# Performance work log

Hardware: AMD Instinct MI355X
Metric: run time of the kernel (lower is better)

Reference implementation:

```python
import jax, jax.numpy as jnp
import numpy as np

D_MODEL = 2048
D_FF = 8192


def _act_quant(x):
    # BitNet b1.58 per-token int8 absmax activation quantization with STE passthrough
    scale = 127.0 / jnp.clip(jnp.max(jnp.abs(x), axis=-1, keepdims=True), 1e-5)
    xq = jnp.clip(jnp.round(x * scale), -128.0, 127.0) / scale
    return x + jax.lax.stop_gradient(xq - x)


def _weight_quant(w):
    # Ternary {-1,0,1} weight quantization with per-tensor mean-abs scale
    scale = 1.0 / jnp.clip(jnp.mean(jnp.abs(w)), 1e-5)
    wq = jnp.clip(jnp.round(w * scale), -1.0, 1.0) / scale
    return w + jax.lax.stop_gradient(wq - w)


def _bitlinear(x, w):
    # y = Q_act(x) @ Q_w(w)^T   (w has shape [out, in], torch Linear convention)
    return jnp.einsum('bsd,fd->bsf', _act_quant(x), _weight_quant(w))


def setup_inputs() -> dict:
    key = jax.random.key(0)
    k_x, k_w1, k_w2 = jax.random.split(key, 3)
    x = jax.random.normal(k_x, (4, 4096, D_MODEL), dtype=jnp.float32)
    # torch Linear default init scale ~ 1/sqrt(fan_in)
    W1 = jax.random.normal(k_w1, (D_FF, D_MODEL), dtype=jnp.float32) / np.sqrt(D_MODEL)
    W2 = jax.random.normal(k_w2, (D_MODEL, D_FF), dtype=jnp.float32) / np.sqrt(D_FF)
    return {"x": x, "W1": W1, "W2": W2}


def reference(x, W1, W2):
    h = jax.nn.silu(_bitlinear(x, W1))   # [B, S, d_ff]
    return _bitlinear(h, W2)             # [B, S, d_model]; dropout p=0 -> identity
```

## Files before the change

### kernel.cpp

```cpp
#include <hip/hip_runtime.h>
#include <hip/hip_bf16.h>
#include <cstdint>

#define DM 2048
#define DF 8192

typedef int v4i __attribute__((ext_vector_type(4)));
typedef short v8s __attribute__((ext_vector_type(8)));

__device__ __forceinline__ float silu_f(float y) {
  return y * (1.0f / (1.0f + expf(-y)));
}

__device__ __forceinline__ void gload_lds16(const void* g, void* l) {
  __builtin_amdgcn_global_load_lds(
      (const __attribute__((address_space(1))) void*)g,
      (__attribute__((address_space(3))) void*)l, 16, 0, 0);
}

__global__ __launch_bounds__(256) void abs_sum_k(const float* __restrict__ w,
                                                 float* __restrict__ partial) {
  const int t = threadIdx.x;
  const float4* wp = (const float4*)w;
  const long base = (long)blockIdx.x * 4096;
  float s = 0.f;
#pragma unroll
  for (int i = 0; i < 16; ++i) {
    float4 v = wp[base + i * 256 + t];
    s += fabsf(v.x) + fabsf(v.y) + fabsf(v.z) + fabsf(v.w);
  }
#pragma unroll
  for (int d = 1; d < 64; d <<= 1) s += __shfl_xor(s, d, 64);
  __shared__ float wsum[4];
  if ((t & 63) == 0) wsum[t >> 6] = s;
  __syncthreads();
  if (t == 0) partial[blockIdx.x] = (wsum[0] + wsum[1]) + (wsum[2] + wsum[3]);
}

__global__ __launch_bounds__(256) void finalize_scales_k(const float* __restrict__ p1,
                                                         const float* __restrict__ p2,
                                                         float* __restrict__ sc) {
  const float* p = (blockIdx.x == 0) ? p1 : p2;
  const int t = threadIdx.x;
  float s = (p[t] + p[t + 256]) + (p[t + 512] + p[t + 768]);
#pragma unroll
  for (int d = 1; d < 64; d <<= 1) s += __shfl_xor(s, d, 64);
  __shared__ float wsum[4];
  if ((t & 63) == 0) wsum[t >> 6] = s;
  __syncthreads();
  if (t == 0) {
    float total = (wsum[0] + wsum[1]) + (wsum[2] + wsum[3]);
    float mean = total * (1.0f / 16777216.0f);
    float c = fmaxf(mean, 1e-5f);
    sc[blockIdx.x * 2 + 0] = 1.0f / c;
    sc[blockIdx.x * 2 + 1] = c;
  }
}

__global__ __launch_bounds__(256) void tern_quant_k(const float* __restrict__ w,
                                                    int8_t* __restrict__ wq,
                                                    const float* __restrict__ scp) {
  const float s = scp[0];
  const long i = (long)blockIdx.x * 256 + threadIdx.x;
  float4 v = ((const float4*)w)[i];
  int q0 = (int)rintf(v.x * s); q0 = q0 < -1 ? -1 : (q0 > 1 ? 1 : q0);
  int q1 = (int)rintf(v.y * s); q1 = q1 < -1 ? -1 : (q1 > 1 ? 1 : q1);
  int q2 = (int)rintf(v.z * s); q2 = q2 < -1 ? -1 : (q2 > 1 ? 1 : q2);
  int q3 = (int)rintf(v.w * s); q3 = q3 < -1 ? -1 : (q3 > 1 ? 1 : q3);
  ((int*)wq)[i] = (q0 & 255) | ((q1 & 255) << 8) | ((q2 & 255) << 16) | ((q3 & 255) << 24);
}

__global__ __launch_bounds__(256) void act_quant_x_k(const float* __restrict__ x,
                                                     int8_t* __restrict__ xq,
                                                     float* __restrict__ inv_sx) {
  const int t = threadIdx.x;
  const long row = blockIdx.x;
  const float4* xr = (const float4*)(x + row * DM);
  float4 v0 = xr[t * 2], v1 = xr[t * 2 + 1];
  float m = fmaxf(fmaxf(fmaxf(fabsf(v0.x), fabsf(v0.y)), fmaxf(fabsf(v0.z), fabsf(v0.w))),
                  fmaxf(fmaxf(fabsf(v1.x), fabsf(v1.y)), fmaxf(fabsf(v1.z), fabsf(v1.w))));
#pragma unroll
  for (int d = 1; d < 64; d <<= 1) m = fmaxf(m, __shfl_xor(m, d, 64));
  __shared__ float wm[4];
  if ((t & 63) == 0) wm[t >> 6] = m;
  __syncthreads();
  m = fmaxf(fmaxf(wm[0], wm[1]), fmaxf(wm[2], wm[3]));
  const float scale = 127.0f / fmaxf(m, 1e-5f);
  if (t == 0) inv_sx[row] = 1.0f / scale;
  float vv[8] = {v0.x, v0.y, v0.z, v0.w, v1.x, v1.y, v1.z, v1.w};
  int q[8];
#pragma unroll
  for (int j = 0; j < 8; ++j) {
    int qq = (int)rintf(vv[j] * scale);
    q[j] = qq < -128 ? -128 : (qq > 127 ? 127 : qq);
  }
  int lo = (q[0] & 255) | ((q[1] & 255) << 8) | ((q[2] & 255) << 16) | ((q[3] & 255) << 24);
  int hi = (q[4] & 255) | ((q[5] & 255) << 8) | ((q[6] & 255) << 16) | ((q[7] & 255) << 24);
  ((int2*)(xq + row * DM))[t] = make_int2(lo, hi);
}

template <int MO, int NO>
__device__ __forceinline__ void cluster(const v4i (&af)[4][2], const v4i (&bf)[2][2],
                                        v4i (&acc)[8][4]) {
  __builtin_amdgcn_s_setprio(1);
#pragma unroll
  for (int ks = 0; ks < 2; ++ks)
#pragma unroll
    for (int m = 0; m < 4; ++m)
#pragma unroll
      for (int n = 0; n < 2; ++n)
        acc[MO + m][NO + n] = __builtin_amdgcn_mfma_i32_16x16x64_i8(
            af[m][ks], bf[n][ks], acc[MO + m][NO + n], 0, 0, 0);
  __builtin_amdgcn_s_setprio(0);
}

template <int K, int N, int EPI>
__global__ __launch_bounds__(512, 2) void gemm8_i8_k(
    const int8_t* __restrict__ A, const int8_t* __restrict__ B,
    const float* __restrict__ rowInv, const float* __restrict__ invswp,
    short* __restrict__ Y16, float* __restrict__ Out) {
  constexpr int NT = K / 128;
  constexpr int NBX = N / 256;
  __shared__ __align__(16) uint8_t lds[131072];

  const int t = threadIdx.x;
  const int wave = t >> 6;
  const int lane = t & 63;
  const int wr = wave >> 2;
  const int wc = wave & 3;
  const int l15 = lane & 15, l4 = lane >> 4;

  const int cpx = (int)gridDim.x >> 3;
  const int bid0 = blockIdx.x;
  const int bid = (bid0 & 7) * cpx + (bid0 >> 3);
  const int bx = bid % NBX, by = bid / NBX;
  const long arow0 = (long)by * 256;
  const long bcol0 = (long)bx * 256;

  const int8_t* Ablk = A + arow0 * K;
  const int8_t* Bblk = B + bcol0 * K;

  const int srow = t >> 3;
  const int scol = ((t & 7) ^ (srow & 7)) << 4;

  const int rAo = (wr * 128 + l15) * 128;
  const int rBo = (wc * 64 + l15) * 128;
  const int sw = (l15 & 7) << 4;
  const int cc0 = (l4 * 16) ^ sw;
  const int cc1 = (64 | (l4 * 16)) ^ sw;

  v4i acc[8][4] = {};
  v4i a_lo[4][2], a_hi[4][2], b_lo[2][2], b_hi[2][2];

#define STAGE(ktile_, part_)                                                      \
  do {                                                                            \
    const int kk = (ktile_);                                                      \
    if (kk < NT) {                                                                \
      uint8_t* d0 = lds + ((kk & 1) << 16) + ((part_) << 14) + (wave << 10);      \
      const int8_t* sp = ((part_) < 2) ? Ablk : Bblk;                             \
      const int8_t* s0 =                                                          \
          sp + (long)((((part_) & 1) << 7) + srow) * K + ((long)kk << 7) + scol;  \
      gload_lds16(s0, d0);                                                        \
      gload_lds16(s0 + ((long)K << 6), d0 + 8192);                                \
    }                                                                             \
  } while (0)

#define FENCE       asm volatile("" ::: "memory")
#define WAIT_LGKM0  asm volatile("s_waitcnt lgkmcnt(0)"  ::: "memory")
#define WAIT_VM4    asm volatile("s_waitcnt vmcnt(4)"    ::: "memory")
#define WAIT_VM0    asm volatile("s_waitcnt vmcnt(0)"    ::: "memory")

  STAGE(0, 0); STAGE(0, 1); STAGE(0, 2); STAGE(0, 3);
  STAGE(1, 0); STAGE(1, 1);
  WAIT_VM4;
  __builtin_amdgcn_s_barrier();
  FENCE;
  {
    const uint8_t* sA0 = lds;
#pragma unroll
    for (int m = 0; m < 4; ++m) {
      a_lo[m][0] = *(const v4i*)(sA0 + rAo + m * 2048 + cc0);
      a_lo[m][1] = *(const v4i*)(sA0 + rAo + m * 2048 + cc1);
    }
  }

  for (int kt = 0; kt < NT; ++kt) {
    const uint8_t* sA = lds + ((kt & 1) << 16);
    const uint8_t* sB = sA + 32768;
    const uint8_t* sAn = lds + (((kt + 1) & 1) << 16);

#pragma unroll
    for (int n = 0; n < 2; ++n) {
      b_lo[n][0] = *(const v4i*)(sB + rBo + n * 2048 + cc0);
      b_lo[n][1] = *(const v4i*)(sB + rBo + n * 2048 + cc1);
    }
#pragma unroll
    for (int n = 0; n < 2; ++n) {
      b_hi[n][0] = *(const v4i*)(sB + rBo + (n + 2) * 2048 + cc0);
      b_hi[n][1] = *(const v4i*)(sB + rBo + (n + 2) * 2048 + cc1);
    }
#pragma unroll
    for (int m = 0; m < 4; ++m) {
      a_hi[m][0] = *(const v4i*)(sA + rAo + (m + 4) * 2048 + cc0);
      a_hi[m][1] = *(const v4i*)(sA + rAo + (m + 4) * 2048 + cc1);
    }
    STAGE(kt + 1, 2);
    STAGE(kt + 1, 3);
    cluster<0, 0>(a_lo, b_lo, acc);
    cluster<0, 2>(a_lo, b_hi, acc);
    WAIT_VM4;
    WAIT_LGKM0;
    __builtin_amdgcn_s_barrier();
    FENCE;
    if (kt + 1 < NT) {
#pragma unroll
      for (int m = 0; m < 4; ++m) {
        a_lo[m][0] = *(const v4i*)(sAn + rAo + m * 2048 + cc0);
        a_lo[m][1] = *(const v4i*)(sAn + rAo + m * 2048 + cc1);
      }
    }
    STAGE(kt + 2, 0);
    STAGE(kt + 2, 1);
    cluster<4, 0>(a_hi, b_lo, acc);
    cluster<4, 2>(a_hi, b_hi, acc);
    if (kt < NT - 2) {
      WAIT_VM4;
    } else {
      WAIT_VM0;
    }
    __builtin_amdgcn_s_barrier();
    FENCE;
  }

  if constexpr (EPI == 1) {
    __syncthreads();
#pragma unroll
    for (int mi = 0; mi < 8; ++mi) {
#pragma unroll
      for (int r = 0; r < 4; ++r) {
        const int row = wr * 128 + mi * 16 + l4 * 4 + r;
#pragma unroll
        for (int ni = 0; ni < 4; ++ni) {
          int yi = acc[mi][ni][r];
          int ys = yi < -32767 ? -32767 : (yi > 32767 ? 32767 : yi);
          const int col = wc * 64 + ni * 16 + l15;
          *(short*)(lds + ((row * 512 + col * 2) ^ ((row & 7) << 4))) = (short)ys;
        }
      }
    }
    __syncthreads();
    const int row = t >> 1;
    const int half = t & 1;
    short* gp = Y16 + (arow0 + row) * (long)DF + bcol0 + half * 128;
#pragma unroll
    for (int i = 0; i < 16; ++i) {
      v8s yv = *(const v8s*)(lds + ((row * 512 + half * 256 + i * 16) ^ ((row & 7) << 4)));
      *(v8s*)(gp + i * 8) = yv;
    }
  } else {
    const float invsw = invswp[0];
#pragma unroll
    for (int mi = 0; mi < 8; ++mi) {
#pragma unroll
      for (int r = 0; r < 4; ++r) {
        const long grow = arow0 + wr * 128 + mi * 16 + l4 * 4 + r;
        const float c2 = rowInv[grow] * invsw;
#pragma unroll
        for (int ni = 0; ni < 4; ++ni)
          Out[grow * N + bcol0 + wc * 64 + ni * 16 + l15] = (float)acc[mi][ni][r] * c2;
      }
    }
  }
#undef STAGE
#undef FENCE
#undef WAIT_LGKM0
#undef WAIT_VM4
#undef WAIT_VM0
}

__global__ __launch_bounds__(256) void quant_h_k(const short* __restrict__ Y16,
                                                 const float* __restrict__ inv_sx,
                                                 const float* __restrict__ sc,
                                                 int8_t* __restrict__ hq,
                                                 float* __restrict__ inv_sh) {
  const int t = threadIdx.x;
  const long row = blockIdx.x;
  const float c1 = inv_sx[row] * sc[1];
  const v8s* yp = (const v8s*)(Y16 + row * DF);
  float h[32];
  float mx = 0.f;
#pragma unroll
  for (int b = 0; b < 4; ++b) {
    v8s s8 = yp[b * 256 + t];
#pragma unroll
    for (int j = 0; j < 8; ++j) {
      float hv = silu_f((float)s8[j] * c1);
      h[b * 8 + j] = hv;
      mx = fmaxf(mx, fabsf(hv));
    }
  }
#pragma unroll
  for (int d = 1; d < 64; d <<= 1) mx = fmaxf(mx, __shfl_xor(mx, d, 64));
  __shared__ float wm[4];
  if ((t & 63) == 0) wm[t >> 6] = mx;
  __syncthreads();
  const float m = fmaxf(fmaxf(wm[0], wm[1]), fmaxf(wm[2], wm[3]));
  const float scale = 127.0f / fmaxf(m, 1e-5f);
  if (t == 0) inv_sh[row] = 1.0f / scale;
  int2* op = (int2*)(hq + row * DF);
#pragma unroll
  for (int b = 0; b < 4; ++b) {
    int q[8];
#pragma unroll
    for (int j = 0; j < 8; ++j) {
      int qq = (int)rintf(h[b * 8 + j] * scale);
      q[j] = qq < -128 ? -128 : (qq > 127 ? 127 : qq);
    }
    int lo = (q[0] & 255) | ((q[1] & 255) << 8) | ((q[2] & 255) << 16) | ((q[3] & 255) << 24);
    int hi = (q[4] & 255) | ((q[5] & 255) << 8) | ((q[6] & 255) << 16) | ((q[7] & 255) << 24);
    op[b * 256 + t] = make_int2(lo, hi);
  }
}

extern "C" void kernel_launch(void* const* d_in, const int* in_sizes, int n_in,
                              void* d_out, int out_size, void* d_ws, size_t ws_size,
                              hipStream_t stream) {
  const float* x = (const float*)d_in[0];
  const float* W1 = (const float*)d_in[1];
  const float* W2 = (const float*)d_in[2];
  float* out = (float*)d_out;

  uint8_t* w = (uint8_t*)d_ws;
  float* sc = (float*)(w + 0);
  float* p1 = (float*)(w + 256);
  float* p2 = (float*)(w + 256 + 4096);
  float* inv_sx = (float*)(w + 8448);
  float* inv_sh = (float*)(w + 8448 + 65536);
  uint8_t* w1q = w + 8448 + 131072 + 4194304;
  uint8_t* w2q = w1q + 16777216;
  uint8_t* xq = w2q + 16777216;
  uint8_t* hq = xq + 33554432;
  short* y16 = (short*)(hq + 134217728);

  abs_sum_k<<<1024, 256, 0, stream>>>(W1, p1);
  abs_sum_k<<<1024, 256, 0, stream>>>(W2, p2);
  finalize_scales_k<<<2, 256, 0, stream>>>(p1, p2, sc);
  tern_quant_k<<<16384, 256, 0, stream>>>(W1, (int8_t*)w1q, sc + 0);
  tern_quant_k<<<16384, 256, 0, stream>>>(W2, (int8_t*)w2q, sc + 2);
  act_quant_x_k<<<16384, 256, 0, stream>>>(x, (int8_t*)xq, inv_sx);
  gemm8_i8_k<2048, 8192, 1><<<2048, 512, 0, stream>>>(
      (const int8_t*)xq, (const int8_t*)w1q, nullptr, nullptr, y16, nullptr);
  quant_h_k<<<16384, 256, 0, stream>>>(y16, inv_sx, sc, (int8_t*)hq, inv_sh);
  gemm8_i8_k<8192, 2048, 0><<<512, 512, 0, stream>>>(
      (const int8_t*)hq, (const int8_t*)w2q, inv_sh, sc + 3, nullptr, out);
}
```

Baseline: 765.2 us.

## Load B fragments directly from global into registers, stage only A in LDS

The int8 GEMM now stages only the A tile through LDS and has each wave load its B (weight) fragments straight from global memory into registers, prefetching the next k-tile during the MFMA clusters. Block ordering is flipped so consecutive blocks share the same B column tile, which favours cache reuse of the weights. The main loop has one barrier per k-tile instead of two and the vmcnt thresholds are adjusted to match. This removes LDS traffic and writes for B, at the cost of uncoalesced 16-byte global loads per lane and more register pressure.

```diff
diff --git a/kernel.cpp b/kernel.cpp
--- a/kernel.cpp
+++ b/kernel.cpp
@@ -115,12 +115,12 @@
 }
 
 template <int K, int N, int EPI>
-__global__ __launch_bounds__(512, 2) void gemm8_i8_k(
+__global__ __launch_bounds__(512, 2) void gemmbd_i8_k(
     const int8_t* __restrict__ A, const int8_t* __restrict__ B,
     const float* __restrict__ rowInv, const float* __restrict__ invswp,
     short* __restrict__ Y16, float* __restrict__ Out) {
   constexpr int NT = K / 128;
-  constexpr int NBX = N / 256;
+  constexpr int NBY = 64;
   __shared__ __align__(16) uint8_t lds[131072];
 
   const int t = threadIdx.x;
@@ -133,101 +133,93 @@
   const int cpx = (int)gridDim.x >> 3;
   const int bid0 = blockIdx.x;
   const int bid = (bid0 & 7) * cpx + (bid0 >> 3);
-  const int bx = bid % NBX, by = bid / NBX;
+  const int by = bid % NBY, bx = bid / NBY;
   const long arow0 = (long)by * 256;
   const long bcol0 = (long)bx * 256;
 
   const int8_t* Ablk = A + arow0 * K;
-  const int8_t* Bblk = B + bcol0 * K;
 
   const int srow = t >> 3;
   const int scol = ((t & 7) ^ (srow & 7)) << 4;
 
   const int rAo = (wr * 128 + l15) * 128;
-  const int rBo = (wc * 64 + l15) * 128;
   const int sw = (l15 & 7) << 4;
   const int cc0 = (l4 * 16) ^ sw;
   const int cc1 = (64 | (l4 * 16)) ^ sw;
 
+  const int8_t* Bfrag = B + (bcol0 + wc * 64 + l15) * (long)K + l4 * 16;
+
   v4i acc[8][4] = {};
   v4i a_lo[4][2], a_hi[4][2], b_lo[2][2], b_hi[2][2];
 
-#define STAGE(ktile_, part_)                                                      \
+#define STAGEA(ktile_, part_)                                                     \
   do {                                                                            \
     const int kk = (ktile_);                                                      \
     if (kk < NT) {                                                                \
-      uint8_t* d0 = lds + ((kk & 1) << 16) + ((part_) << 14) + (wave << 10);      \
-      const int8_t* sp = ((part_) < 2) ? Ablk : Bblk;                             \
+      uint8_t* d0 = lds + ((kk & 1) << 15) + ((part_) << 14) + (wave << 10);      \
       const int8_t* s0 =                                                          \
-          sp + (long)((((part_) & 1) << 7) + srow) * K + ((long)kk << 7) + scol;  \
+          Ablk + (long)(((part_) << 7) + srow) * K + ((long)kk << 7) + scol;      \
       gload_lds16(s0, d0);                                                        \
       gload_lds16(s0 + ((long)K << 6), d0 + 8192);                                \
     }                                                                             \
   } while (0)
 
+#define LOAD_BLO(kk_)                                                             \
+  _Pragma("unroll")                                                               \
+  for (int n = 0; n < 2; ++n) {                                                   \
+    b_lo[n][0] = *(const v4i*)(Bfrag + (long)n * 16 * K + ((long)(kk_) << 7));    \
+    b_lo[n][1] = *(const v4i*)(Bfrag + (long)n * 16 * K + ((long)(kk_) << 7) + 64); \
+  }
+
+#define LOAD_BHI(kk_)                                                             \
+  _Pragma("unroll")                                                               \
+  for (int n = 0; n < 2; ++n) {                                                   \
+    b_hi[n][0] = *(const v4i*)(Bfrag + (long)(n + 2) * 16 * K + ((long)(kk_) << 7)); \
+    b_hi[n][1] = *(const v4i*)(Bfrag + (long)(n + 2) * 16 * K + ((long)(kk_) << 7) + 64); \
+  }
+
 #define FENCE       asm volatile("" ::: "memory")
 #define WAIT_LGKM0  asm volatile("s_waitcnt lgkmcnt(0)"  ::: "memory")
-#define WAIT_VM4    asm volatile("s_waitcnt vmcnt(4)"    ::: "memory")
+#define WAIT_VM8    asm volatile("s_waitcnt vmcnt(8)"    ::: "memory")
 #define WAIT_VM0    asm volatile("s_waitcnt vmcnt(0)"    ::: "memory")
 
-  STAGE(0, 0); STAGE(0, 1); STAGE(0, 2); STAGE(0, 3);
-  STAGE(1, 0); STAGE(1, 1);
-  WAIT_VM4;
+  STAGEA(0, 0); STAGEA(0, 1);
+  FENCE;
+  LOAD_BLO(0);
+  LOAD_BHI(0);
+  WAIT_VM8;
   __builtin_amdgcn_s_barrier();
   FENCE;
-  {
-    const uint8_t* sA0 = lds;
+
+  for (int kt = 0; kt < NT; ++kt) {
+    STAGEA(kt + 1, 0);
+    STAGEA(kt + 1, 1);
+    FENCE;
+
+    const uint8_t* sA = lds + ((kt & 1) << 15);
 #pragma unroll
     for (int m = 0; m < 4; ++m) {
-      a_lo[m][0] = *(const v4i*)(sA0 + rAo + m * 2048 + cc0);
-      a_lo[m][1] = *(const v4i*)(sA0 + rAo + m * 2048 + cc1);
-    }
-  }
-
-  for (int kt = 0; kt < NT; ++kt) {
-    const uint8_t* sA = lds + ((kt & 1) << 16);
-    const uint8_t* sB = sA + 32768;
-    const uint8_t* sAn = lds + (((kt + 1) & 1) << 16);
-
-#pragma unroll
-    for (int n = 0; n < 2; ++n) {
-      b_lo[n][0] = *(const v4i*)(sB + rBo + n * 2048 + cc0);
-      b_lo[n][1] = *(const v4i*)(sB + rBo + n * 2048 + cc1);
-    }
-#pragma unroll
-    for (int n = 0; n < 2; ++n) {
-      b_hi[n][0] = *(const v4i*)(sB + rBo + (n + 2) * 2048 + cc0);
-      b_hi[n][1] = *(const v4i*)(sB + rBo + (n + 2) * 2048 + cc1);
+      a_lo[m][0] = *(const v4i*)(sA + rAo + m * 2048 + cc0);
+      a_lo[m][1] = *(const v4i*)(sA + rAo + m * 2048 + cc1);
     }
 #pragma unroll
     for (int m = 0; m < 4; ++m) {
       a_hi[m][0] = *(const v4i*)(sA + rAo + (m + 4) * 2048 + cc0);
       a_hi[m][1] = *(const v4i*)(sA + rAo + (m + 4) * 2048 + cc1);
     }
-    STAGE(kt + 1, 2);
-    STAGE(kt + 1, 3);
+
     cluster<0, 0>(a_lo, b_lo, acc);
+    cluster<4, 0>(a_hi, b_lo, acc);
+    if (kt + 1 < NT) { LOAD_BLO(kt + 1); }
     cluster<0, 2>(a_lo, b_hi, acc);
-    WAIT_VM4;
-    WAIT_LGKM0;
-    __builtin_amdgcn_s_barrier();
-    FENCE;
+    cluster<4, 2>(a_hi, b_hi, acc);
     if (kt + 1 < NT) {
-#pragma unroll
-      for (int m = 0; m < 4; ++m) {
-        a_lo[m][0] = *(const v4i*)(sAn + rAo + m * 2048 + cc0);
-        a_lo[m][1] = *(const v4i*)(sAn + rAo + m * 2048 + cc1);
-      }
-    }
-    STAGE(kt + 2, 0);
-    STAGE(kt + 2, 1);
-    cluster<4, 0>(a_hi, b_lo, acc);
-    cluster<4, 2>(a_hi, b_hi, acc);
-    if (kt < NT - 2) {
-      WAIT_VM4;
+      LOAD_BHI(kt + 1);
+      WAIT_VM8;
     } else {
       WAIT_VM0;
     }
+    WAIT_LGKM0;
     __builtin_amdgcn_s_barrier();
     FENCE;
   }
@@ -271,10 +263,12 @@
       }
     }
   }
-#undef STAGE
+#undef STAGEA
+#undef LOAD_BLO
+#undef LOAD_BHI
 #undef FENCE
 #undef WAIT_LGKM0
-#undef WAIT_VM4
+#undef WAIT_VM8
 #undef WAIT_VM0
 }
 
@@ -348,9 +342,9 @@
   tern_quant_k<<<16384, 256, 0, stream>>>(W1, (int8_t*)w1q, sc + 0);
   tern_quant_k<<<16384, 256, 0, stream>>>(W2, (int8_t*)w2q, sc + 2);
   act_quant_x_k<<<16384, 256, 0, stream>>>(x, (int8_t*)xq, inv_sx);
-  gemm8_i8_k<2048, 8192, 1><<<2048, 512, 0, stream>>>(
+  gemmbd_i8_k<2048, 8192, 1><<<2048, 512, 0, stream>>>(
       (const int8_t*)xq, (const int8_t*)w1q, nullptr, nullptr, y16, nullptr);
   quant_h_k<<<16384, 256, 0, stream>>>(y16, inv_sx, sc, (int8_t*)hq, inv_sh);
-  gemm8_i8_k<8192, 2048, 0><<<512, 512, 0, stream>>>(
+  gemmbd_i8_k<8192, 2048, 0><<<512, 512, 0, stream>>>(
       (const int8_t*)hq, (const int8_t*)w2q, inv_sh, sc + 3, nullptr, out);
 }
```

Measured after the change: 1.164 ms. 52.1% more time.
